# Performance work log

Measured on AMD Instinct MI355X. Metric: run time of the kernel, lower is better.

Reference implementation:

```python
import jax, jax.numpy as jnp
import numpy as np

N_HEAD, D_MODEL, D_HEAD = 16, 1024, 64
SEQ, BATCH = 2048, 2
EPS = 1e-5


def layer_norm(x, g, b):
    mu = jnp.mean(x, axis=-1, keepdims=True)
    var = jnp.var(x, axis=-1, keepdims=True)
    return (x - mu) * jax.lax.rsqrt(var + EPS) * g + b


def pos_table(n_rows, d_model):
    pos = jnp.arange(n_rows, dtype=jnp.float32)[:, None]
    freqs = jnp.power(10000.0, -jnp.arange(0, d_model, 2, dtype=jnp.float32) / d_model)
    ang = pos * freqs  # [n_rows, d_model//2]
    tab = jnp.zeros((n_rows, d_model), dtype=jnp.float32)
    tab = tab.at[:, 0::2].set(jnp.sin(ang))
    tab = tab.at[:, 1::2].set(jnp.cos(ang))
    return tab


def setup_inputs() -> dict:
    key = jax.random.key(0)
    ks = jax.random.split(key, 7)
    s = 0.02
    return {
        "dec_inp": jax.random.normal(ks[0], (SEQ, BATCH, D_MODEL), jnp.float32),
        "Wq": jax.random.normal(ks[1], (N_HEAD * D_HEAD, D_MODEL), jnp.float32) * s,
        "Wkv": jax.random.normal(ks[2], (2 * N_HEAD * D_HEAD, D_MODEL), jnp.float32) * s,
        "Wo": jax.random.normal(ks[3], (D_MODEL, N_HEAD * D_HEAD), jnp.float32) * s,
        "g1": jnp.ones((D_MODEL,), jnp.float32),
        "b1": jnp.zeros((D_MODEL,), jnp.float32),
        "Wff": jax.random.normal(ks[4], (D_MODEL, N_HEAD * D_HEAD), jnp.float32) * s,
        "g2": jnp.ones((D_MODEL,), jnp.float32),
        "b2": jnp.zeros((D_MODEL,), jnp.float32),
    }


def reference(dec_inp, Wq, Wkv, Wo, g1, b1, Wff, g2, b2):
    S, B, D = dec_inp.shape
    scale = 1.0 / (D_HEAD ** 0.5)
    # projections (post-lnorm path, no mems: c == h)
    q = jnp.einsum('ibd,ed->ibe', dec_inp, Wq).reshape(S, B, N_HEAD, D_HEAD)
    kv = jnp.einsum('ibd,ed->ibe', dec_inp, Wkv)
    k, v = jnp.split(kv, 2, axis=-1)
    k = k.reshape(S, B, N_HEAD, D_HEAD)
    v = v.reshape(S, B, N_HEAD, D_HEAD)
    # attention: scores [i, j, b, n], softmax over j (dim=1)
    scores = jnp.einsum('ibnd,jbnd->ijbn', q, k) * scale
    prob = jax.nn.softmax(scores, axis=1)
    vec = jnp.einsum('ijbn,jbnd->ibnd', prob, v).reshape(S, B, N_HEAD * D_HEAD)
    attn_out = jnp.einsum('ibe,de->ibd', vec, Wo)
    out = layer_norm(dec_inp + attn_out, g1, b1)
    # output += ff(output)
    out = out + jnp.einsum('ibe,de->ibd', out, Wff)
    out = layer_norm(out, g2, b2)
    # output += pos_emb(output)  ==  2*out + pe  (pe indexed by shape[1]==batch)
    pe = pos_table(B, D)  # [B, D], broadcasts over seq
    return out + (out + pe)
```

## Files before the change

kernel.cpp:

```cpp
#include <hip/hip_runtime.h>
#include <hip/hip_bf16.h>
#include <math.h>


typedef __bf16 bf16x8 __attribute__((ext_vector_type(8)));
typedef float f32x4  __attribute__((ext_vector_type(4)));

typedef const __attribute__((address_space(1))) unsigned int as1_uint;
typedef __attribute__((address_space(3))) unsigned int as3_uint;

constexpr int S_SEQ = 2048;
constexpr int DH    = 64;
constexpr float C1SC = 0.125f * 1.44269504088896f;

#define WS_MB (1ull << 20)

__device__ __forceinline__ void gload16(void* lds, const void* g) {
  __builtin_amdgcn_global_load_lds((as1_uint*)g, (as3_uint*)lds, 16, 0, 0);
}

__device__ __forceinline__ float fast_exp2(float x) {
  float r;
  asm volatile("v_exp_f32 %0, %1\n\ts_nop 1" : "=v"(r) : "v"(x));
  return r;
}
__device__ __forceinline__ unsigned cvt_pk_bf16(float lo, float hi) {
  unsigned r;
  asm("v_cvt_pk_bf16_f32 %0, %1, %2" : "=v"(r) : "v"(lo), "v"(hi));
  return r;
}

__device__ __forceinline__ void cvt4(const float* __restrict__ in,
                                     __hip_bfloat16* __restrict__ out, int idx) {
  float4 v = ((const float4*)in)[idx];
  uint2 p;
  p.x = cvt_pk_bf16(v.x, v.y);
  p.y = cvt_pk_bf16(v.z, v.w);
  *(uint2*)(out + (size_t)idx * 4) = p;
}

__global__ __launch_bounds__(256)
void prep_kernel(const float* __restrict__ x, const float* __restrict__ Wq,
                 const float* __restrict__ Wkv, const float* __restrict__ Wo,
                 const float* __restrict__ Wff,
                 __hip_bfloat16* __restrict__ Xb,
                 __hip_bfloat16* __restrict__ Wqkv_b,
                 __hip_bfloat16* __restrict__ Wo_b,
                 __hip_bfloat16* __restrict__ Wff_b,
                 float* __restrict__ pe) {
  const int bid = blockIdx.x, t = threadIdx.x;
  if (bid < 4096) {
    cvt4(x, Xb, bid * 256 + t);
  } else if (bid < 5120) {
    cvt4(Wq, Wqkv_b, (bid - 4096) * 256 + t);
  } else if (bid < 7168) {
    cvt4(Wkv, Wqkv_b + 1024 * 1024, (bid - 5120) * 256 + t);
  } else if (bid < 8192) {
    cvt4(Wo, Wo_b, (bid - 7168) * 256 + t);
  } else if (bid < 9216) {
    cvt4(Wff, Wff_b, (bid - 8192) * 256 + t);
  } else {
#pragma unroll
    for (int rep = 0; rep < 2; ++rep) {
      const int k = rep * 256 + t;
      float freq = expf(-(2.0f * (float)k / 1024.0f) * logf(10000.0f));
      pe[2 * k]            = 0.0f;
      pe[2 * k + 1]        = 1.0f;
      pe[1024 + 2 * k]     = sinf(freq);
      pe[1024 + 2 * k + 1] = cosf(freq);
    }
  }
}

template <int MODE, int BN>
__global__ __launch_bounds__(256)
void gemm_bt(const __hip_bfloat16* __restrict__ A,
             const __hip_bfloat16* __restrict__ Bw,
             float* __restrict__ C,
             __hip_bfloat16* __restrict__ Qb,
             __hip_bfloat16* __restrict__ Kb,
             __hip_bfloat16* __restrict__ VTb,
             int Ndim, int Kdim) {
  constexpr int ASZ = 128 * 64 * 2;
  constexpr int BSZ = BN * 64 * 2;
  constexpr int NI  = BN / 32;
  __shared__ __align__(16) char smem[2 * (ASZ + BSZ)];
  const int t = threadIdx.x, w = t >> 6, l = t & 63;
  const int bm = blockIdx.y * 128, bn = blockIdx.x * BN;
  const int m0 = (w >> 1) * 64, n0 = (w & 1) * (BN / 2);
  const int lrow = l >> 3, lcol = l & 7;
  const int ll = l & 15, lg = l >> 4;
  const int scol = (lcol ^ lrow) * 8;

  auto stage = [&](char* buf, int kt) {
#pragma unroll
    for (int r = 0; r < 4; ++r) {
      const int chunk = r * 4 + w;
      const int row = chunk * 8 + lrow;
      gload16(buf + chunk * 1024 + l * 16,
              A + (size_t)(bm + row) * Kdim + kt + scol);
    }
#pragma unroll
    for (int r = 0; r < BN / 32; ++r) {
      const int chunk = r * 4 + w;
      const int row = chunk * 8 + lrow;
      gload16(buf + ASZ + chunk * 1024 + l * 16,
              Bw + (size_t)(bn + row) * Kdim + kt + scol);
    }
  };

  f32x4 acc[4][NI] = {};

  stage(smem, 0);
  stage(smem + (ASZ + BSZ), 64);
  const int NST = Kdim / 64;
  for (int kt = 0; kt < NST; ++kt) {
    if (kt < NST - 1) {
      if constexpr (BN == 128)
        asm volatile("s_waitcnt vmcnt(8)" ::: "memory");
      else
        asm volatile("s_waitcnt vmcnt(6)" ::: "memory");
    } else {
      asm volatile("s_waitcnt vmcnt(0)" ::: "memory");
    }
    __builtin_amdgcn_s_barrier();
    char* sA = smem + (kt & 1) * (ASZ + BSZ);
    const char* sB = sA + ASZ;
#pragma unroll
    for (int ks = 0; ks < 2; ++ks) {
      bf16x8 a[4], bfr[NI];
#pragma unroll
      for (int mi = 0; mi < 4; ++mi) {
        const int row = m0 + mi * 16 + ll;
        a[mi] = *(const bf16x8*)(sA + row * 128 +
                                 (((ks * 4 + lg) ^ (ll & 7)) << 4));
      }
#pragma unroll
      for (int ni = 0; ni < NI; ++ni) {
        const int row = n0 + ni * 16 + ll;
        bfr[ni] = *(const bf16x8*)(sB + row * 128 +
                                   (((ks * 4 + lg) ^ (ll & 7)) << 4));
      }
#pragma unroll
      for (int mi = 0; mi < 4; ++mi)
#pragma unroll
        for (int ni = 0; ni < NI; ++ni)
          acc[mi][ni] = __builtin_amdgcn_mfma_f32_16x16x32_bf16(
              a[mi], bfr[ni], acc[mi][ni], 0, 0, 0);
    }
    if (kt + 2 < NST) {
      __builtin_amdgcn_s_barrier();
      stage(sA, (kt + 2) * 64);
    }
  }

  if (MODE == 0) {
#pragma unroll
    for (int mi = 0; mi < 4; ++mi)
#pragma unroll
      for (int ni = 0; ni < NI; ++ni)
#pragma unroll
        for (int r = 0; r < 4; ++r) {
          const int gm = bm + m0 + mi * 16 + lg * 4 + r;
          const int gn = bn + n0 + ni * 16 + ll;
          C[(size_t)gm * Ndim + gn] = acc[mi][ni][r];
        }
  } else {
    __syncthreads();
    __hip_bfloat16* img = (__hip_bfloat16*)smem;
    const bool isV = (bn >= 2048);
    const float qsc = (bn < 1024) ? C1SC : 1.0f;
#pragma unroll
    for (int mi = 0; mi < 4; ++mi)
#pragma unroll
      for (int ni = 0; ni < NI; ++ni)
#pragma unroll
        for (int r = 0; r < 4; ++r) {
          const int gml = m0 + mi * 16 + lg * 4 + r;
          const int gnl = n0 + ni * 16 + ll;
          const int off = isV ? gnl * 136 + ((gml & 1) << 6) + (gml >> 1)
                              : gml * 136 + gnl;
          img[off] = __float2bfloat16(acc[mi][ni][r] * qsc);
        }
    __syncthreads();
    const int i0 = bm >> 1;
    const int tile0 = bm >> 6;
#pragma unroll
    for (int j = 0; j < 8; ++j) {
      const int c = j * 256 + t;
      uint4 val;
      __hip_bfloat16* dst;
      if (bn < 1024) {
        const int bb = c >> 10, hl = (c >> 9) & 1;
        const int q = c & 511, il = q >> 3, dh0 = (q & 7) * 8;
        val = *(const uint4*)&img[(il * 2 + bb) * 136 + hl * 64 + dh0];
        dst = Qb + ((size_t)(bb * 16 + (bn >> 6) + hl) * 2048 + i0 + il) * 64 + dh0;
      } else if (bn < 2048) {
        const int run = c >> 6, lane = c & 63;
        const int bb = run >> 4, hl = (run >> 3) & 1, th = (run >> 2) & 1,
                  instr = run & 3;
        const int lg2 = lane >> 4, ll2 = lane & 15;
        const int r32 = (ll2 >> 2) * 8 + (ll2 & 3) + ((instr >> 1) << 2);
        const int il = th * 32 + r32;
        const int dh0 = (instr & 1) * 32 + lg2 * 8;
        val = *(const uint4*)&img[(il * 2 + bb) * 136 + hl * 64 + dh0];
        dst = Kb + (size_t)(bb * 16 + ((bn - 1024) >> 6) + hl) * 131072 +
              (size_t)(tile0 + th) * 2048 + instr * 512 + lane * 8;
      } else {
        const int run = c >> 6, lane = c & 63;
        const int bb = run >> 4, hl = (run >> 3) & 1, th = (run >> 2) & 1,
                  df = run & 3;
        const int lg2 = lane >> 4, ll2 = lane & 15;
        const int il0 = th * 32 + lg2 * 8;
        const int gnl = hl * 64 + df * 16 + ll2;
        val = *(const uint4*)&img[gnl * 136 + bb * 64 + il0];
        dst = VTb + (size_t)(bb * 16 + ((bn - 2048) >> 6) + hl) * 131072 +
              (size_t)(tile0 + th) * 2048 + df * 512 + lane * 8;
      }
      *(uint4*)dst = val;
    }
  }
}


#define MFMA_B16 __builtin_amdgcn_mfma_f32_16x16x32_bf16

#define STAGE2(bufp, cb)                                                      \
  {                                                                           \
    gload16((bufp) + woff, Kf + (cb) + wl16);                                 \
    gload16((bufp) + 4096 + woff, Vf + (cb) + wl16);                          \
    gload16((bufp) + 8192 + woff, Kf + (cb) + 4096 + wl16);                   \
    gload16((bufp) + 12288 + woff, Vf + (cb) + 4096 + wl16);                  \
  }

#define COMPUTE2(curA)                                                        \
  {                                                                           \
    bf16x8 kkA[4], vvA[4], kkB[4], vvB[4];                                    \
    _Pragma("unroll")                                                         \
    for (int i = 0; i < 4; ++i) {                                             \
      kkA[i] = *(const bf16x8*)((curA) + i * 1024 + l16);                     \
      vvA[i] = *(const bf16x8*)((curA) + 4096 + i * 1024 + l16);              \
      kkB[i] = *(const bf16x8*)((curA) + 8192 + i * 1024 + l16);              \
      vvB[i] = *(const bf16x8*)((curA) + 12288 + i * 1024 + l16);             \
    }                                                                         \
    const f32x4 z = {0.f, 0.f, 0.f, 0.f};                                     \
    f32x4 sA0[2], sA1[2], sB0[2], sB1[2];                                     \
    __builtin_amdgcn_s_setprio(1);                                            \
    _Pragma("unroll")                                                         \
    for (int qi = 0; qi < 2; ++qi) {                                          \
      sA0[qi] = MFMA_B16(kkA[0], qf[qi][0], z, 0, 0, 0);                      \
      sA1[qi] = MFMA_B16(kkA[2], qf[qi][0], z, 0, 0, 0);                      \
      sB0[qi] = MFMA_B16(kkB[0], qf[qi][0], z, 0, 0, 0);                      \
      sB1[qi] = MFMA_B16(kkB[2], qf[qi][0], z, 0, 0, 0);                      \
      sA0[qi] = MFMA_B16(kkA[1], qf[qi][1], sA0[qi], 0, 0, 0);                \
      sA1[qi] = MFMA_B16(kkA[3], qf[qi][1], sA1[qi], 0, 0, 0);                \
      sB0[qi] = MFMA_B16(kkB[1], qf[qi][1], sB0[qi], 0, 0, 0);                \
      sB1[qi] = MFMA_B16(kkB[3], qf[qi][1], sB1[qi], 0, 0, 0);                \
    }                                                                         \
    __builtin_amdgcn_s_setprio(0);                                            \
    union { unsigned u[4]; bf16x8 v; } pkA[2], pkB[2];                        \
    _Pragma("unroll")                                                         \
    for (int qi = 0; qi < 2; ++qi) {                                          \
      float pA[8], pB[8];                                                     \
      _Pragma("unroll")                                                       \
      for (int r = 0; r < 4; ++r) {                                           \
        pA[r]     = fast_exp2(sA0[qi][r]);                                    \
        pA[4 + r] = fast_exp2(sA1[qi][r]);                                    \
        pB[r]     = fast_exp2(sB0[qi][r]);                                    \
        pB[4 + r] = fast_exp2(sB1[qi][r]);                                    \
      }                                                                       \
      pkA[qi].u[0] = cvt_pk_bf16(pA[0], pA[1]);                               \
      pkA[qi].u[1] = cvt_pk_bf16(pA[2], pA[3]);                               \
      pkA[qi].u[2] = cvt_pk_bf16(pA[4], pA[5]);                               \
      pkA[qi].u[3] = cvt_pk_bf16(pA[6], pA[7]);                               \
      pkB[qi].u[0] = cvt_pk_bf16(pB[0], pB[1]);                               \
      pkB[qi].u[1] = cvt_pk_bf16(pB[2], pB[3]);                               \
      pkB[qi].u[2] = cvt_pk_bf16(pB[4], pB[5]);                               \
      pkB[qi].u[3] = cvt_pk_bf16(pB[6], pB[7]);                               \
    }                                                                         \
    __builtin_amdgcn_s_setprio(1);                                            \
    _Pragma("unroll")                                                         \
    for (int qi = 0; qi < 2; ++qi) {                                          \
      _Pragma("unroll")                                                       \
      for (int df = 0; df < 4; ++df) {                                        \
        oacc[qi][df] = MFMA_B16(pkA[qi].v, vvA[df], oacc[qi][df], 0, 0, 0);   \
        oacc[qi][df] = MFMA_B16(pkB[qi].v, vvB[df], oacc[qi][df], 0, 0, 0);   \
      }                                                                       \
      oaccS[qi] = MFMA_B16(pkA[qi].v, onesv.v, oaccS[qi], 0, 0, 0);           \
      oaccS[qi] = MFMA_B16(pkB[qi].v, onesv.v, oaccS[qi], 0, 0, 0);           \
    }                                                                         \
    __builtin_amdgcn_s_setprio(0);                                            \
  }

#define PHASE(curbuf, stgbuf, stgoff, vmN_, doStage_)                         \
  {                                                                           \
    asm volatile("s_waitcnt vmcnt(" #vmN_ ")" ::: "memory");                  \
    __builtin_amdgcn_s_barrier();                                             \
    if (doStage_) STAGE2(stgbuf, stgoff);                                     \
    COMPUTE2(curbuf);                                                         \
  }

__global__ __launch_bounds__(256)
void attn_kernel(const __hip_bfloat16* __restrict__ Qb,
                 const __hip_bfloat16* __restrict__ Kb,
                 const __hip_bfloat16* __restrict__ VTb,
                 __hip_bfloat16* __restrict__ vec) {
  __shared__ __align__(16) char lds[3 * 16384];
  const int t = threadIdx.x, w = t >> 6, l = t & 63;
  const int bid = blockIdx.x;
  const int slot = bid >> 3;
  const int bh = (bid & 7) * 4 + (slot & 3);
  const int qt = slot >> 2;
  const int b = bh >> 4, h = bh & 15;
  const __hip_bfloat16* Q = Qb + (size_t)bh * S_SEQ * DH;
  const char* Kf = (const char*)Kb + (size_t)bh * 262144;
  const char* Vf = (const char*)VTb + (size_t)bh * 262144;
  const int ll = l & 15, lg = l >> 4;
  const int l16 = l * 16;
  const int woff = w * 1024 + l16;
  const int wl16 = woff;

  const int qbase = qt * 128 + w * 32;
  bf16x8 qf[2][2];
#pragma unroll
  for (int qi = 0; qi < 2; ++qi) {
    qf[qi][0] = *(const bf16x8*)(Q + (size_t)(qbase + qi * 16 + ll) * 64 + lg * 8);
    qf[qi][1] = *(const bf16x8*)(Q + (size_t)(qbase + qi * 16 + ll) * 64 + 32 + lg * 8);
  }

  union { unsigned u[4]; bf16x8 v; } onesv;
  onesv.u[0] = 0x3F803F80u; onesv.u[1] = 0x3F803F80u;
  onesv.u[2] = 0x3F803F80u; onesv.u[3] = 0x3F803F80u;

  f32x4 oacc[2][4] = {};
  f32x4 oaccS[2] = {};

  char* b0 = lds;
  char* b1 = lds + 16384;
  char* b2 = lds + 32768;

  STAGE2(b0, 0);
  STAGE2(b1, 8192);

  int cb = 2 * 8192;
  for (int i = 0; i < 10; ++i) {
    PHASE(b0, b2, cb, 4, true); cb += 8192;
    PHASE(b1, b0, cb, 4, true); cb += 8192;
    PHASE(b2, b1, cb, 4, true); cb += 8192;
  }
  PHASE(b0, b2, 0, 4, false);
  PHASE(b1, b0, 0, 0, false);

#pragma unroll
  for (int qi = 0; qi < 2; ++qi) {
    float invR[4];
#pragma unroll
    for (int r = 0; r < 4; ++r) invR[r] = 1.0f / oaccS[qi][r];
#pragma unroll
    for (int df = 0; df < 4; ++df)
#pragma unroll
      for (int r = 0; r < 4; ++r) {
        const int row = qbase + qi * 16 + 4 * lg + r;
        const int e = h * 64 + df * 16 + ll;
        vec[((size_t)row * 2 + b) * 1024 + e] =
            __float2bfloat16(oacc[qi][df][r] * invR[r]);
      }
  }
}

__global__ __launch_bounds__(256)
void add_ln_kernel(const float* __restrict__ X, const float* __restrict__ Yadd,
                   const float* __restrict__ g, const float* __restrict__ bb,
                   float* __restrict__ out_f32,
                   __hip_bfloat16* __restrict__ out_b16) {
  const int row = blockIdx.x, t = threadIdx.x;
  const float4 x4 = *(const float4*)(X + (size_t)row * 1024 + t * 4);
  const float4 a4 = *(const float4*)(Yadd + (size_t)row * 1024 + t * 4);
  float v[4] = {x4.x + a4.x, x4.y + a4.y, x4.z + a4.z, x4.w + a4.w};
  float s = v[0] + v[1] + v[2] + v[3];
  float s2 = v[0] * v[0] + v[1] * v[1] + v[2] * v[2] + v[3] * v[3];
#pragma unroll
  for (int off = 1; off < 64; off <<= 1) {
    s += __shfl_xor(s, off);
    s2 += __shfl_xor(s2, off);
  }
  __shared__ float rs[4], rs2[4];
  if ((t & 63) == 0) { rs[t >> 6] = s; rs2[t >> 6] = s2; }
  __syncthreads();
  const float tot = rs[0] + rs[1] + rs[2] + rs[3];
  const float tot2 = rs2[0] + rs2[1] + rs2[2] + rs2[3];
  const float mu = tot * (1.0f / 1024.0f);
  const float var = tot2 * (1.0f / 1024.0f) - mu * mu;
  const float rstd = rsqrtf(var + 1e-5f);
  const float4 g4 = *(const float4*)(g + t * 4);
  const float4 b4 = *(const float4*)(bb + t * 4);
  float y[4];
  y[0] = (v[0] - mu) * rstd * g4.x + b4.x;
  y[1] = (v[1] - mu) * rstd * g4.y + b4.y;
  y[2] = (v[2] - mu) * rstd * g4.z + b4.z;
  y[3] = (v[3] - mu) * rstd * g4.w + b4.w;
  *(float4*)(out_f32 + (size_t)row * 1024 + t * 4) =
      make_float4(y[0], y[1], y[2], y[3]);
  uint2 pk2;
  pk2.x = cvt_pk_bf16(y[0], y[1]);
  pk2.y = cvt_pk_bf16(y[2], y[3]);
  *(uint2*)(out_b16 + (size_t)row * 1024 + t * 4) = pk2;
}

__global__ __launch_bounds__(256)
void final_kernel(const float* __restrict__ X, const float* __restrict__ Yadd,
                  const float* __restrict__ g, const float* __restrict__ bb,
                  const float* __restrict__ pe, float* __restrict__ out) {
  const int row = blockIdx.x, t = threadIdx.x;
  const float4 x4 = *(const float4*)(X + (size_t)row * 1024 + t * 4);
  const float4 a4 = *(const float4*)(Yadd + (size_t)row * 1024 + t * 4);
  float v[4] = {x4.x + a4.x, x4.y + a4.y, x4.z + a4.z, x4.w + a4.w};
  float s = v[0] + v[1] + v[2] + v[3];
  float s2 = v[0] * v[0] + v[1] * v[1] + v[2] * v[2] + v[3] * v[3];
#pragma unroll
  for (int off = 1; off < 64; off <<= 1) {
    s += __shfl_xor(s, off);
    s2 += __shfl_xor(s2, off);
  }
  __shared__ float rs[4], rs2[4];
  if ((t & 63) == 0) { rs[t >> 6] = s; rs2[t >> 6] = s2; }
  __syncthreads();
  const float tot = rs[0] + rs[1] + rs[2] + rs[3];
  const float tot2 = rs2[0] + rs2[1] + rs2[2] + rs2[3];
  const float mu = tot * (1.0f / 1024.0f);
  const float var = tot2 * (1.0f / 1024.0f) - mu * mu;
  const float rstd = rsqrtf(var + 1e-5f);
  const float4 g4 = *(const float4*)(g + t * 4);
  const float4 b4 = *(const float4*)(bb + t * 4);
  const int bidx = row & 1;
  const float4 p4 = *(const float4*)(pe + bidx * 1024 + t * 4);
  float y[4];
  y[0] = 2.0f * ((v[0] - mu) * rstd * g4.x + b4.x) + p4.x;
  y[1] = 2.0f * ((v[1] - mu) * rstd * g4.y + b4.y) + p4.y;
  y[2] = 2.0f * ((v[2] - mu) * rstd * g4.z + b4.z) + p4.z;
  y[3] = 2.0f * ((v[3] - mu) * rstd * g4.w + b4.w) + p4.w;
  *(float4*)(out + (size_t)row * 1024 + t * 4) = make_float4(y[0], y[1], y[2], y[3]);
}

extern "C" void kernel_launch(void* const* d_in, const int* in_sizes, int n_in,
                              void* d_out, int out_size, void* d_ws,
                              size_t ws_size, hipStream_t stream) {
  const float* x   = (const float*)d_in[0];
  const float* Wq  = (const float*)d_in[1];
  const float* Wkv = (const float*)d_in[2];
  const float* Wo  = (const float*)d_in[3];
  const float* g1  = (const float*)d_in[4];
  const float* b1  = (const float*)d_in[5];
  const float* Wff = (const float*)d_in[6];
  const float* g2  = (const float*)d_in[7];
  const float* b2  = (const float*)d_in[8];

  char* ws = (char*)d_ws;
  __hip_bfloat16* Wqkv_b = (__hip_bfloat16*)(ws + 0);
  __hip_bfloat16* Wo_b   = (__hip_bfloat16*)(ws + 6 * WS_MB);
  __hip_bfloat16* Wff_b  = (__hip_bfloat16*)(ws + 8 * WS_MB);
  __hip_bfloat16* Xb     = (__hip_bfloat16*)(ws + 10 * WS_MB);
  __hip_bfloat16* Qb     = (__hip_bfloat16*)(ws + 18 * WS_MB);
  __hip_bfloat16* Kb     = (__hip_bfloat16*)(ws + 26 * WS_MB);
  __hip_bfloat16* VTb    = (__hip_bfloat16*)(ws + 34 * WS_MB);
  __hip_bfloat16* vecb   = (__hip_bfloat16*)(ws + 42 * WS_MB);
  float* attn            = (float*)(ws + 18 * WS_MB);
  float* out1            = (float*)(ws + 50 * WS_MB);
  __hip_bfloat16* out1b  = (__hip_bfloat16*)(ws + 66 * WS_MB);
  float* ffb             = (float*)(ws + 34 * WS_MB);
  float* pe              = (float*)(ws + 74 * WS_MB);

  prep_kernel<<<9217, 256, 0, stream>>>(x, Wq, Wkv, Wo, Wff, Xb, Wqkv_b,
                                        Wo_b, Wff_b, pe);
  gemm_bt<1, 128><<<dim3(24, 32), 256, 0, stream>>>(Xb, Wqkv_b, nullptr, Qb,
                                                    Kb, VTb, 3072, 1024);
  attn_kernel<<<dim3(512), 256, 0, stream>>>(Qb, Kb, VTb, vecb);
  gemm_bt<0, 64><<<dim3(16, 32), 256, 0, stream>>>(vecb, Wo_b, attn, nullptr,
                                                   nullptr, nullptr, 1024, 1024);
  add_ln_kernel<<<4096, 256, 0, stream>>>(x, attn, g1, b1, out1, out1b);
  gemm_bt<0, 64><<<dim3(16, 32), 256, 0, stream>>>(out1b, Wff_b, ffb, nullptr,
                                                   nullptr, nullptr, 1024, 1024);
  final_kernel<<<4096, 256, 0, stream>>>(out1, ffb, g2, b2, pe, (float*)d_out);
}
```

Before: 137.5 us.

## Load V fragments directly from global memory, staging only K through LDS

V tiles no longer go through the triple-buffered LDS pipeline; each wave reads its V fragments straight from global memory into registers at the start of each phase. Only K is staged through LDS, which halves the shared-memory footprint (48 KB to 24 KB) and can allow more blocks per CU. The vmcnt thresholds are adjusted for the two K loads per stage. In exchange, V loads are issued without any prefetch, so their global/L2 latency can sit directly in front of the PV MFMAs.

Measured after the change: 139.9 us. Within noise of the previous version (+1.8%).

```diff
diff --git a/kernel.cpp b/kernel.cpp
--- a/kernel.cpp
+++ b/kernel.cpp
@@ -225,24 +225,25 @@
 
 #define MFMA_B16 __builtin_amdgcn_mfma_f32_16x16x32_bf16
 
-#define STAGE2(bufp, cb)                                                      \
+#define STAGEK(bufp, cb)                                                      \
   {                                                                           \
     gload16((bufp) + woff, Kf + (cb) + wl16);                                 \
-    gload16((bufp) + 4096 + woff, Vf + (cb) + wl16);                          \
-    gload16((bufp) + 8192 + woff, Kf + (cb) + 4096 + wl16);                   \
-    gload16((bufp) + 12288 + woff, Vf + (cb) + 4096 + wl16);                  \
-  }
-
-#define COMPUTE2(curA)                                                        \
+    gload16((bufp) + 4096 + woff, Kf + (cb) + 4096 + wl16);                   \
+  }
+
+#define PHASE(curbuf, stgbuf, stgoff, cbv, vmN_, doStage_)                    \
   {                                                                           \
+    asm volatile("s_waitcnt vmcnt(" #vmN_ ")" ::: "memory");                  \
+    __builtin_amdgcn_s_barrier();                                             \
     bf16x8 kkA[4], vvA[4], kkB[4], vvB[4];                                    \
     _Pragma("unroll")                                                         \
     for (int i = 0; i < 4; ++i) {                                             \
-      kkA[i] = *(const bf16x8*)((curA) + i * 1024 + l16);                     \
-      vvA[i] = *(const bf16x8*)((curA) + 4096 + i * 1024 + l16);              \
-      kkB[i] = *(const bf16x8*)((curA) + 8192 + i * 1024 + l16);              \
-      vvB[i] = *(const bf16x8*)((curA) + 12288 + i * 1024 + l16);             \
+      kkA[i] = *(const bf16x8*)((curbuf) + i * 1024 + l16);                   \
+      kkB[i] = *(const bf16x8*)((curbuf) + 4096 + i * 1024 + l16);            \
+      vvA[i] = *(const bf16x8*)(Vf + (cbv) + i * 1024 + l16);                 \
+      vvB[i] = *(const bf16x8*)(Vf + (cbv) + 4096 + i * 1024 + l16);          \
     }                                                                         \
+    if (doStage_) STAGEK(stgbuf, stgoff);                                     \
     const f32x4 z = {0.f, 0.f, 0.f, 0.f};                                     \
     f32x4 sA0[2], sA1[2], sB0[2], sB1[2];                                     \
     __builtin_amdgcn_s_setprio(1);                                            \
@@ -292,20 +293,12 @@
     __builtin_amdgcn_s_setprio(0);                                            \
   }
 
-#define PHASE(curbuf, stgbuf, stgoff, vmN_, doStage_)                         \
-  {                                                                           \
-    asm volatile("s_waitcnt vmcnt(" #vmN_ ")" ::: "memory");                  \
-    __builtin_amdgcn_s_barrier();                                             \
-    if (doStage_) STAGE2(stgbuf, stgoff);                                     \
-    COMPUTE2(curbuf);                                                         \
-  }
-
 __global__ __launch_bounds__(256)
 void attn_kernel(const __hip_bfloat16* __restrict__ Qb,
                  const __hip_bfloat16* __restrict__ Kb,
                  const __hip_bfloat16* __restrict__ VTb,
                  __hip_bfloat16* __restrict__ vec) {
-  __shared__ __align__(16) char lds[3 * 16384];
+  __shared__ __align__(16) char lds[3 * 8192];
   const int t = threadIdx.x, w = t >> 6, l = t & 63;
   const int bid = blockIdx.x;
   const int slot = bid >> 3;
@@ -336,20 +329,21 @@
   f32x4 oaccS[2] = {};
 
   char* b0 = lds;
-  char* b1 = lds + 16384;
-  char* b2 = lds + 32768;
-
-  STAGE2(b0, 0);
-  STAGE2(b1, 8192);
+  char* b1 = lds + 8192;
+  char* b2 = lds + 16384;
+
+  STAGEK(b0, 0);
+  STAGEK(b1, 8192);
 
   int cb = 2 * 8192;
+  int cbv = 0;
   for (int i = 0; i < 10; ++i) {
-    PHASE(b0, b2, cb, 4, true); cb += 8192;
-    PHASE(b1, b0, cb, 4, true); cb += 8192;
-    PHASE(b2, b1, cb, 4, true); cb += 8192;
-  }
-  PHASE(b0, b2, 0, 4, false);
-  PHASE(b1, b0, 0, 0, false);
+    PHASE(b0, b2, cb, cbv, 2, true); cb += 8192; cbv += 8192;
+    PHASE(b1, b0, cb, cbv, 2, true); cb += 8192; cbv += 8192;
+    PHASE(b2, b1, cb, cbv, 2, true); cb += 8192; cbv += 8192;
+  }
+  PHASE(b0, b2, 0, 30 * 8192, 2, false);
+  PHASE(b1, b0, 0, 31 * 8192, 0, false);
 
 #pragma unroll
   for (int qi = 0; qi < 2; ++qi) {
```
